# Performance work log

Hardware: AMD Instinct MI355X
Metric: run time of the kernel (lower is better)

The kernel has to match this reference:

```python
import jax, jax.numpy as jnp
import numpy as np

N_EMBD = 384
N_HEAD = 6
HEAD_SIZE = N_EMBD // N_HEAD
D_FF = 4 * N_EMBD
LN_EPS = 1e-3  # keras LayerNormalization default epsilon


def setup_inputs() -> dict:
    key = jax.random.key(0)
    ks = jax.random.split(key, 12)
    B, T = 4, 2048
    s = 1.0 / np.sqrt(N_EMBD)
    return {
        "x": jax.random.normal(ks[0], (B, T, N_EMBD), dtype=jnp.float32),
        "Wq": jax.random.normal(ks[1], (N_EMBD, N_EMBD), dtype=jnp.float32) * s,
        "Wk": jax.random.normal(ks[2], (N_EMBD, N_EMBD), dtype=jnp.float32) * s,
        "Wv": jax.random.normal(ks[3], (N_EMBD, N_EMBD), dtype=jnp.float32) * s,
        "Wo": jax.random.normal(ks[4], (N_EMBD, N_EMBD), dtype=jnp.float32) * s,
        "bo": jnp.zeros((N_EMBD,), dtype=jnp.float32),
        "W1": jax.random.normal(ks[5], (N_EMBD, D_FF), dtype=jnp.float32) * s,
        "b1": jnp.zeros((D_FF,), dtype=jnp.float32),
        "W2": jax.random.normal(ks[6], (D_FF, N_EMBD), dtype=jnp.float32) * (1.0 / np.sqrt(D_FF)),
        "b2": jnp.zeros((N_EMBD,), dtype=jnp.float32),
        "g1": jnp.ones((N_EMBD,), dtype=jnp.float32),
        "be1": jnp.zeros((N_EMBD,), dtype=jnp.float32),
        "g2": jnp.ones((N_EMBD,), dtype=jnp.float32),
        "be2": jnp.zeros((N_EMBD,), dtype=jnp.float32),
    }


def _layer_norm(x, gamma, beta):
    mu = jnp.mean(x, axis=-1, keepdims=True)
    var = jnp.mean(jnp.square(x - mu), axis=-1, keepdims=True)
    return (x - mu) * jax.lax.rsqrt(var + LN_EPS) * gamma + beta


def _block(x, Wq, Wk, Wv, Wo, bo, W1, b1, W2, b2, g1, be1, g2, be2):
    B, T, C = x.shape
    H, D = N_HEAD, HEAD_SIZE
    q = (x @ Wq).reshape(B, T, H, D).transpose(0, 2, 1, 3)  # [B,H,T,D]
    k = (x @ Wk).reshape(B, T, H, D).transpose(0, 2, 1, 3)
    v = (x @ Wv).reshape(B, T, H, D).transpose(0, 2, 1, 3)
    scores = jnp.einsum("bhqd,bhkd->bhqk", q, k) / jnp.sqrt(jnp.float32(D))
    causal = jnp.tril(jnp.ones((T, T), dtype=bool))
    scores = jnp.where(causal, scores, jnp.float32(-1e9))
    attn = jax.nn.softmax(scores, axis=-1)  # dropout is identity at inference
    out = jnp.einsum("bhqk,bhkd->bhqd", attn, v)
    out = out.transpose(0, 2, 1, 3).reshape(B, T, H * D)
    y = out @ Wo + bo
    x = _layer_norm(x + y, g1, be1)
    y = jax.nn.relu(x @ W1 + b1) @ W2 + b2
    return _layer_norm(x + y, g2, be2)


def reference(x, Wq, Wk, Wv, Wo, bo, W1, b1, W2, b2, g1, be1, g2, be2):
    return _block(x, Wq, Wk, Wv, Wo, bo, W1, b1, W2, b2, g1, be1, g2, be2)
```

## Files before the change

kernel.cpp:

```cpp
#include <hip/hip_runtime.h>

#define C_DIM  384
#define HEADS  6
#define HD     64
#define FF_DIM 1536
#define LN_EPS 1e-3f
#define TSEQ   2048
#define BATCH  4
#define LOG2E  1.4426950408889634f

typedef __attribute__((ext_vector_type(4))) float          f32x4;
typedef __attribute__((ext_vector_type(4))) float          float4_t;
typedef __attribute__((ext_vector_type(8))) short          bfrag;
typedef __attribute__((ext_vector_type(4))) unsigned short ushort4_t;
typedef __attribute__((ext_vector_type(8))) unsigned short ushort8_t;

__device__ inline unsigned short f2bf(float f) {
    unsigned int u = __builtin_bit_cast(unsigned int, f);
    u += 0x7fff + ((u >> 16) & 1);
    return (unsigned short)(u >> 16);
}

__device__ inline void gload_lds16(const void* g, void* l) {
    __builtin_amdgcn_global_load_lds(
        (const __attribute__((address_space(1))) unsigned int*)g,
        (__attribute__((address_space(3))) unsigned int*)l,
        16, 0, 0);
}

__global__ __launch_bounds__(256)
void transpose_w4(const float* __restrict__ Wq, const float* __restrict__ Wk,
                  const float* __restrict__ Wv, const float* __restrict__ Wo,
                  unsigned short* __restrict__ Dq, unsigned short* __restrict__ Dk,
                  unsigned short* __restrict__ Dv, unsigned short* __restrict__ Do_)
{
    __shared__ float tile[32][33];
    const int z = blockIdx.z;
    const float* W = z == 0 ? Wq : (z == 1 ? Wk : (z == 2 ? Wv : Wo));
    unsigned short* D = z == 0 ? Dq : (z == 1 ? Dk : (z == 2 ? Dv : Do_));
    const int tx = threadIdx.x, ty = threadIdx.y;
    const int n0 = blockIdx.x * 32, k0 = blockIdx.y * 32;
    #pragma unroll
    for (int i = 0; i < 32; i += 8)
        tile[ty + i][tx] = W[(size_t)(k0 + ty + i) * C_DIM + n0 + tx];
    __syncthreads();
    #pragma unroll
    for (int i = 0; i < 32; i += 8)
        D[(size_t)(n0 + ty + i) * C_DIM + k0 + tx] = f2bf(tile[tx][ty + i]);
}

__global__ __launch_bounds__(256)
void transpose_w(const float* __restrict__ W, unsigned short* __restrict__ Wt, int K, int N)
{
    __shared__ float tile[32][33];
    const int tx = threadIdx.x, ty = threadIdx.y;
    const int n0 = blockIdx.x * 32, k0 = blockIdx.y * 32;
    #pragma unroll
    for (int i = 0; i < 32; i += 8)
        tile[ty + i][tx] = W[(size_t)(k0 + ty + i) * N + n0 + tx];
    __syncthreads();
    #pragma unroll
    for (int i = 0; i < 32; i += 8)
        Wt[(size_t)(n0 + ty + i) * K + k0 + tx] = f2bf(tile[tx][ty + i]);
}

__global__ __launch_bounds__(256)
void cvt_f32_bf16_x4(const float* __restrict__ in, unsigned short* __restrict__ out, int n4)
{
    int i = blockIdx.x * 256 + threadIdx.x;
    if (i >= n4) return;
    float4_t v = ((const float4_t*)in)[i];
    ushort4_t o = { f2bf(v.x), f2bf(v.y), f2bf(v.z), f2bf(v.w) };
    ((ushort4_t*)out)[i] = o;
}

__global__ __launch_bounds__(256)
void vtrans_kernel(const unsigned short* __restrict__ qkv, unsigned short* __restrict__ vt)
{
    __shared__ unsigned short tile[32][34];
    const int tx = threadIdx.x, ty = threadIdx.y;
    const int bh = blockIdx.z, b = bh / HEADS, h = bh % HEADS;
    const int t0 = blockIdx.x * 32, d0 = blockIdx.y * 32;
    #pragma unroll
    for (int i = 0; i < 32; i += 8)
        tile[ty + i][tx] = qkv[(size_t)(b * TSEQ + t0 + ty + i) * 1152 + 2 * C_DIM + h * HD + d0 + tx];
    __syncthreads();
    #pragma unroll
    for (int i = 0; i < 32; i += 8)
        vt[((size_t)bh * HD + d0 + ty + i) * TSEQ + t0 + tx] = tile[tx][ty + i];
}

template<int OBF16, int BIAS, int RELU>
__global__ __launch_bounds__(256)
void gemm_lds(const unsigned short* __restrict__ A, const unsigned short* __restrict__ Bt,
              const float* __restrict__ bias, void* __restrict__ Cv,
              int M, int N, int K)
{
    __shared__ __align__(16) unsigned short As[16 * 512];
    __shared__ __align__(16) unsigned short Bs[16 * 512];

    const int t = threadIdx.x, lane = t & 63, w = t >> 6;
    const int ln16 = lane & 15, hi16 = lane >> 4;
    const int wr = w >> 1, wc = w & 1;
    const int row0 = blockIdx.y * 128, col0 = blockIdx.x * 128;

    f32x4 acc[4][4] = {};

    for (int k0 = 0; k0 < K; k0 += 64) {
        #pragma unroll
        for (int i = 0; i < 4; ++i) {
            const int f  = w * 4 + i;
            const int ks = f >> 3, rf = f & 7;
            const int row = rf * 16 + ln16;
            const int kc  = k0 + ks * 32 + hi16 * 8;
            gload_lds16(&A [(size_t)(row0 + row) * K + kc], &As[f * 512]);
            gload_lds16(&Bt[(size_t)(col0 + row) * K + kc], &Bs[f * 512]);
        }
        __syncthreads();
        #pragma unroll
        for (int ks = 0; ks < 2; ++ks) {
            bfrag a[4], b[4];
            #pragma unroll
            for (int i = 0; i < 4; ++i)
                a[i] = *(const bfrag*)&As[(ks * 8 + wr * 4 + i) * 512 + lane * 8];
            #pragma unroll
            for (int j = 0; j < 4; ++j)
                b[j] = *(const bfrag*)&Bs[(ks * 8 + wc * 4 + j) * 512 + lane * 8];
            #pragma unroll
            for (int i = 0; i < 4; ++i)
                #pragma unroll
                for (int j = 0; j < 4; ++j)
                    acc[i][j] = __builtin_amdgcn_mfma_f32_16x16x32_bf16(a[i], b[j], acc[i][j], 0, 0, 0);
        }
        __syncthreads();
    }

    #pragma unroll
    for (int j = 0; j < 4; ++j) {
        const int col = col0 + wc * 64 + j * 16 + ln16;
        const float bv = BIAS ? bias[col] : 0.0f;
        #pragma unroll
        for (int i = 0; i < 4; ++i) {
            #pragma unroll
            for (int e = 0; e < 4; ++e) {
                const int row = row0 + wr * 64 + i * 16 + hi16 * 4 + e;
                float v = acc[i][j][e] + bv;
                if (RELU) v = fmaxf(v, 0.0f);
                if (OBF16) ((unsigned short*)Cv)[(size_t)row * N + col] = f2bf(v);
                else       ((float*)Cv)[(size_t)row * N + col] = v;
            }
        }
    }
}

__global__ __launch_bounds__(64)
void attn_kernel(const unsigned short* __restrict__ qkv,
                 const unsigned short* __restrict__ vt,
                 unsigned short* __restrict__ att)
{
    __shared__ __align__(16) unsigned short Ps[32][72];
    const int lane = threadIdx.x;
    const int ln16 = lane & 15, hi16 = lane >> 4;
    const int bid = blockIdx.x;
    const int xcd = bid & 7;
    const int i2  = bid >> 3;
    const int bh  = xcd * 3 + (i2 >> 6);
    const int qw  = 63 - (i2 & 63);
    const int b   = bh / HEADS, h = bh % HEADS;
    const int tok0 = qw * 32;
    const size_t qrow0 = (size_t)b * TSEQ;

    bfrag qf[2][2];
    #pragma unroll
    for (int rf = 0; rf < 2; ++rf)
        #pragma unroll
        for (int ks = 0; ks < 2; ++ks)
            qf[rf][ks] = *(const bfrag*)&qkv[(qrow0 + tok0 + rf * 16 + ln16) * 1152 + h * HD + ks * 32 + hi16 * 8];

    f32x4 acc[2][4] = {};
    float mrow[2][4], lrow[2][4];
    #pragma unroll
    for (int rf = 0; rf < 2; ++rf)
        #pragma unroll
        for (int e = 0; e < 4; ++e) { mrow[rf][e] = -1e30f; lrow[rf][e] = 0.0f; }

    const int NT = (qw >> 1) + 1;
    const unsigned short* Kbase = qkv + qrow0 * 1152 + C_DIM + h * HD;
    const unsigned short* Vbase = vt + (size_t)bh * HD * TSEQ;

    bfrag kf[4][2];
    #pragma unroll
    for (int jt = 0; jt < 4; ++jt)
        #pragma unroll
        for (int ks = 0; ks < 2; ++ks)
            kf[jt][ks] = *(const bfrag*)&Kbase[(size_t)(jt * 16 + ln16) * 1152 + ks * 32 + hi16 * 8];

    for (int kt = 0; kt < NT; ++kt) {
        f32x4 sf[2][4] = {};
        #pragma unroll
        for (int jt = 0; jt < 4; ++jt)
            #pragma unroll
            for (int ks = 0; ks < 2; ++ks) {
                sf[0][jt] = __builtin_amdgcn_mfma_f32_16x16x32_bf16(qf[0][ks], kf[jt][ks], sf[0][jt], 0, 0, 0);
                sf[1][jt] = __builtin_amdgcn_mfma_f32_16x16x32_bf16(qf[1][ks], kf[jt][ks], sf[1][jt], 0, 0, 0);
            }

        bfrag vf[4][2];
        #pragma unroll
        for (int dt = 0; dt < 4; ++dt)
            #pragma unroll
            for (int ks = 0; ks < 2; ++ks)
                vf[dt][ks] = *(const bfrag*)&Vbase[(size_t)(dt * 16 + ln16) * TSEQ + kt * 64 + ks * 32 + hi16 * 8];

        const bool last = (kt == NT - 1);
        float p[2][4][4];
        #pragma unroll
        for (int rf = 0; rf < 2; ++rf)
            #pragma unroll
            for (int jt = 0; jt < 4; ++jt)
                #pragma unroll
                for (int e = 0; e < 4; ++e) {
                    float sv = sf[rf][jt][e] * (0.125f * LOG2E);
                    if (last) {
                        const int key = kt * 64 + jt * 16 + ln16;
                        const int row = tok0 + rf * 16 + hi16 * 4 + e;
                        if (key > row) sv = -1e30f;
                    }
                    p[rf][jt][e] = sv;
                }

        float lmax[2][4];
        bool need = false;
        #pragma unroll
        for (int rf = 0; rf < 2; ++rf)
            #pragma unroll
            for (int e = 0; e < 4; ++e) {
                float mx = fmaxf(fmaxf(p[rf][0][e], p[rf][1][e]), fmaxf(p[rf][2][e], p[rf][3][e]));
                lmax[rf][e] = mx;
                need = need || (mx > mrow[rf][e] + 8.0f);
            }
        if (__any(need)) {
            #pragma unroll
            for (int rf = 0; rf < 2; ++rf)
                #pragma unroll
                for (int e = 0; e < 4; ++e) {
                    float rm = lmax[rf][e];
                    rm = fmaxf(rm, __shfl_xor(rm, 1));
                    rm = fmaxf(rm, __shfl_xor(rm, 2));
                    rm = fmaxf(rm, __shfl_xor(rm, 4));
                    rm = fmaxf(rm, __shfl_xor(rm, 8));
                    const float mn = fmaxf(mrow[rf][e], rm);
                    const float corr = exp2f(mrow[rf][e] - mn);
                    mrow[rf][e] = mn;
                    lrow[rf][e] *= corr;
                    #pragma unroll
                    for (int dt = 0; dt < 4; ++dt) acc[rf][dt][e] *= corr;
                }
        }

        if (kt + 1 < NT) {
            const unsigned short* Kn = Kbase + (size_t)(kt + 1) * 64 * 1152;
            #pragma unroll
            for (int jt = 0; jt < 4; ++jt)
                #pragma unroll
                for (int ks = 0; ks < 2; ++ks)
                    kf[jt][ks] = *(const bfrag*)&Kn[(size_t)(jt * 16 + ln16) * 1152 + ks * 32 + hi16 * 8];
        }

        #pragma unroll
        for (int rf = 0; rf < 2; ++rf)
            #pragma unroll
            for (int jt = 0; jt < 4; ++jt)
                #pragma unroll
                for (int e = 0; e < 4; ++e) {
                    const float pe = exp2f(p[rf][jt][e] - mrow[rf][e]);
                    lrow[rf][e] += pe;
                    Ps[rf * 16 + hi16 * 4 + e][jt * 16 + ln16] = f2bf(pe);
                }

        bfrag pf[2][2];
        #pragma unroll
        for (int rf = 0; rf < 2; ++rf)
            #pragma unroll
            for (int ks = 0; ks < 2; ++ks)
                pf[rf][ks] = *(const bfrag*)&Ps[rf * 16 + ln16][ks * 32 + hi16 * 8];
        #pragma unroll
        for (int ks = 0; ks < 2; ++ks)
            #pragma unroll
            for (int rf = 0; rf < 2; ++rf)
                #pragma unroll
                for (int dt = 0; dt < 4; ++dt)
                    acc[rf][dt] = __builtin_amdgcn_mfma_f32_16x16x32_bf16(pf[rf][ks], vf[dt][ks], acc[rf][dt], 0, 0, 0);
    }

    #pragma unroll
    for (int rf = 0; rf < 2; ++rf)
        #pragma unroll
        for (int e = 0; e < 4; ++e) {
            float l = lrow[rf][e];
            l += __shfl_xor(l, 1);
            l += __shfl_xor(l, 2);
            l += __shfl_xor(l, 4);
            l += __shfl_xor(l, 8);
            const float inv = 1.0f / l;
            const size_t row = qrow0 + tok0 + rf * 16 + hi16 * 4 + e;
            #pragma unroll
            for (int dt = 0; dt < 4; ++dt)
                att[row * C_DIM + h * HD + dt * 16 + ln16] = f2bf(acc[rf][dt][e] * inv);
        }
}

template<int WB>
__global__ __launch_bounds__(256)
void ln_residual_kernel(const float* __restrict__ A, const float* __restrict__ R,
                        const float* __restrict__ gamma, const float* __restrict__ beta,
                        float* __restrict__ out, unsigned short* __restrict__ outb, int Mrows)
{
    const int lane = threadIdx.x & 63;
    const int wv   = threadIdx.x >> 6;
    const int row  = blockIdx.x * 4 + wv;
    if (row >= Mrows) return;
    const size_t off = (size_t)row * C_DIM;

    float v[6];
    float sum = 0.0f;
    #pragma unroll
    for (int j = 0; j < 6; ++j) {
        const int c = lane + 64 * j;
        v[j] = A[off + c] + R[off + c];
        sum += v[j];
    }
    #pragma unroll
    for (int o = 1; o < 64; o <<= 1) sum += __shfl_xor(sum, o);
    const float mu = sum * (1.0f / C_DIM);

    float sq = 0.0f;
    #pragma unroll
    for (int j = 0; j < 6; ++j) { const float d = v[j] - mu; sq = fmaf(d, d, sq); }
    #pragma unroll
    for (int o = 1; o < 64; o <<= 1) sq += __shfl_xor(sq, o);
    const float rstd = rsqrtf(sq * (1.0f / C_DIM) + LN_EPS);

    #pragma unroll
    for (int j = 0; j < 6; ++j) {
        const int c = lane + 64 * j;
        const float r = (v[j] - mu) * rstd * gamma[c] + beta[c];
        out[off + c] = r;
        if (WB) outb[off + c] = f2bf(r);
    }
}

extern "C" void kernel_launch(void* const* d_in, const int* in_sizes, int n_in,
                              void* d_out, int out_size, void* d_ws, size_t ws_size,
                              hipStream_t stream)
{
    const float* x   = (const float*)d_in[0];
    const float* Wq  = (const float*)d_in[1];
    const float* Wk  = (const float*)d_in[2];
    const float* Wv  = (const float*)d_in[3];
    const float* Wo  = (const float*)d_in[4];
    const float* bo  = (const float*)d_in[5];
    const float* W1  = (const float*)d_in[6];
    const float* b1  = (const float*)d_in[7];
    const float* W2  = (const float*)d_in[8];
    const float* b2  = (const float*)d_in[9];
    const float* g1  = (const float*)d_in[10];
    const float* be1 = (const float*)d_in[11];
    const float* g2  = (const float*)d_in[12];
    const float* be2 = (const float*)d_in[13];
    float* out = (float*)d_out;

    const int M = BATCH * TSEQ;
    const size_t MC = (size_t)M * C_DIM;

    char* ws = (char*)d_ws;
    unsigned short* qkv = (unsigned short*)ws;
    unsigned short* vt  = (unsigned short*)(ws + (size_t)M*1152*2);
    unsigned short* att = (unsigned short*)(ws + (size_t)M*1152*2 + (size_t)BATCH*HEADS*HD*TSEQ*2);
    unsigned short* h1  = (unsigned short*)ws;
    char* p2 = ws + (size_t)M*1152*2 + (size_t)BATCH*HEADS*HD*TSEQ*2 + MC*2;
    unsigned short* xb  = (unsigned short*)p2;
    float* y   = (float*)(p2 + MC*2);
    float* x1  = (float*)(p2 + MC*2 + MC*4);
    unsigned short* x1b = (unsigned short*)(p2 + MC*2 + 2*MC*4);
    char* p3 = p2 + MC*2 + 2*MC*4 + MC*2;
    unsigned short* Wqkv_t = (unsigned short*)p3;
    unsigned short* Wo_t   = Wqkv_t + (size_t)3*C_DIM*C_DIM;
    unsigned short* W1_t   = Wo_t   + (size_t)C_DIM*C_DIM;
    unsigned short* W2_t   = W1_t   + (size_t)FF_DIM*C_DIM;

    dim3 b256(256), b328(32, 8);

    transpose_w4<<<dim3(C_DIM/32, C_DIM/32, 4), b328, 0, stream>>>(
        Wq, Wk, Wv, Wo,
        Wqkv_t, Wqkv_t + (size_t)C_DIM*C_DIM, Wqkv_t + (size_t)2*C_DIM*C_DIM, Wo_t);
    transpose_w<<<dim3(FF_DIM/32, C_DIM/32), b328, 0, stream>>>(W1, W1_t, C_DIM, FF_DIM);
    transpose_w<<<dim3(C_DIM/32, FF_DIM/32), b328, 0, stream>>>(W2, W2_t, FF_DIM, C_DIM);

    cvt_f32_bf16_x4<<<dim3((MC/4 + 255)/256), b256, 0, stream>>>(x, xb, (int)(MC/4));

    gemm_lds<1, 0, 0><<<dim3(3*C_DIM/128, M/128), b256, 0, stream>>>(
        xb, Wqkv_t, nullptr, qkv, M, 3*C_DIM, C_DIM);

    vtrans_kernel<<<dim3(TSEQ/32, HD/32, BATCH*HEADS), b328, 0, stream>>>(qkv, vt);

    attn_kernel<<<dim3(BATCH*HEADS*64), dim3(64), 0, stream>>>(qkv, vt, att);

    gemm_lds<0, 1, 0><<<dim3(C_DIM/128, M/128), b256, 0, stream>>>(
        att, Wo_t, bo, y, M, C_DIM, C_DIM);

    ln_residual_kernel<1><<<dim3(M/4), b256, 0, stream>>>(x, y, g1, be1, x1, x1b, M);

    gemm_lds<1, 1, 1><<<dim3(FF_DIM/128, M/128), b256, 0, stream>>>(
        x1b, W1_t, b1, h1, M, FF_DIM, C_DIM);

    gemm_lds<0, 1, 0><<<dim3(C_DIM/128, M/128), b256, 0, stream>>>(
        h1, W2_t, b2, y, M, C_DIM, FF_DIM);

    ln_residual_kernel<0><<<dim3(M/4), b256, 0, stream>>>(x1, y, g2, be2, out, nullptr, M);
}
```

Measured before the change: 217.3 us.

## Split causal attention over key chunks and merge partials in a combine kernel

Attention work for each query tile is split into up to four key chunks of eight tiles each, and each chunk runs as its own workgroup. Chunks write unnormalized bf16 partial outputs plus per-row max and sum, and a new combine kernel merges them with log-sum-exp rescaling. This evens out the long causal rows and raises the number of workgroups, at the cost of an extra launch and partial-result traffic. The softmax scale (1/8·log2e) is also folded into the Q columns in the QKV GEMM epilogue, removing a multiply per score.

```diff
diff --git a/kernel.cpp b/kernel.cpp
--- a/kernel.cpp
+++ b/kernel.cpp
@@ -8,6 +8,7 @@
 #define TSEQ   2048
 #define BATCH  4
 #define LOG2E  1.4426950408889634f
+#define QK_SCALE 0.18033688011112042f
 
 typedef __attribute__((ext_vector_type(4))) float          f32x4;
 typedef __attribute__((ext_vector_type(4))) float          float4_t;
@@ -90,7 +91,7 @@
         vt[((size_t)bh * HD + d0 + ty + i) * TSEQ + t0 + tx] = tile[tx][ty + i];
 }
 
-template<int OBF16, int BIAS, int RELU>
+template<int OBF16, int BIAS, int RELU, int QSCALE>
 __global__ __launch_bounds__(256)
 void gemm_lds(const unsigned short* __restrict__ A, const unsigned short* __restrict__ Bt,
               const float* __restrict__ bias, void* __restrict__ Cv,
@@ -139,6 +140,7 @@
     for (int j = 0; j < 4; ++j) {
         const int col = col0 + wc * 64 + j * 16 + ln16;
         const float bv = BIAS ? bias[col] : 0.0f;
+        const float sc = (QSCALE && col < C_DIM) ? QK_SCALE : 1.0f;
         #pragma unroll
         for (int i = 0; i < 4; ++i) {
             #pragma unroll
@@ -146,6 +148,7 @@
                 const int row = row0 + wr * 64 + i * 16 + hi16 * 4 + e;
                 float v = acc[i][j][e] + bv;
                 if (RELU) v = fmaxf(v, 0.0f);
+                if (QSCALE) v *= sc;
                 if (OBF16) ((unsigned short*)Cv)[(size_t)row * N + col] = f2bf(v);
                 else       ((float*)Cv)[(size_t)row * N + col] = v;
             }
@@ -156,16 +159,26 @@
 __global__ __launch_bounds__(64)
 void attn_kernel(const unsigned short* __restrict__ qkv,
                  const unsigned short* __restrict__ vt,
-                 unsigned short* __restrict__ att)
+                 unsigned short* __restrict__ att,
+                 unsigned short* __restrict__ pacc,
+                 float* __restrict__ pml)
 {
     __shared__ __align__(16) unsigned short Ps[32][72];
     const int lane = threadIdx.x;
     const int ln16 = lane & 15, hi16 = lane >> 4;
     const int bid = blockIdx.x;
     const int xcd = bid & 7;
-    const int i2  = bid >> 3;
-    const int bh  = xcd * 3 + (i2 >> 6);
-    const int qw  = 63 - (i2 & 63);
+    const int r   = bid >> 3;
+    const int bh  = xcd * 3 + (r >> 8);
+    const int rr  = r & 255;
+    const int qw  = 63 - (rr >> 2);
+    const int ck  = rr & 3;
+    const int NT  = (qw >> 1) + 1;
+    const int nck = (NT + 7) >> 3;
+    if (ck >= nck) return;
+    const int kt0 = ck * 8;
+    const int kte = min(kt0 + 8, NT);
+
     const int b   = bh / HEADS, h = bh % HEADS;
     const int tok0 = qw * 32;
     const size_t qrow0 = (size_t)b * TSEQ;
@@ -184,7 +197,6 @@
         #pragma unroll
         for (int e = 0; e < 4; ++e) { mrow[rf][e] = -1e30f; lrow[rf][e] = 0.0f; }
 
-    const int NT = (qw >> 1) + 1;
     const unsigned short* Kbase = qkv + qrow0 * 1152 + C_DIM + h * HD;
     const unsigned short* Vbase = vt + (size_t)bh * HD * TSEQ;
 
@@ -193,9 +205,9 @@
     for (int jt = 0; jt < 4; ++jt)
         #pragma unroll
         for (int ks = 0; ks < 2; ++ks)
-            kf[jt][ks] = *(const bfrag*)&Kbase[(size_t)(jt * 16 + ln16) * 1152 + ks * 32 + hi16 * 8];
-
-    for (int kt = 0; kt < NT; ++kt) {
+            kf[jt][ks] = *(const bfrag*)&Kbase[(size_t)(kt0 * 64 + jt * 16 + ln16) * 1152 + ks * 32 + hi16 * 8];
+
+    for (int kt = kt0; kt < kte; ++kt) {
         f32x4 sf[2][4] = {};
         #pragma unroll
         for (int jt = 0; jt < 4; ++jt)
@@ -220,7 +232,7 @@
             for (int jt = 0; jt < 4; ++jt)
                 #pragma unroll
                 for (int e = 0; e < 4; ++e) {
-                    float sv = sf[rf][jt][e] * (0.125f * LOG2E);
+                    float sv = sf[rf][jt][e];
                     if (last) {
                         const int key = kt * 64 + jt * 16 + ln16;
                         const int row = tok0 + rf * 16 + hi16 * 4 + e;
@@ -258,7 +270,7 @@
                 }
         }
 
-        if (kt + 1 < NT) {
+        if (kt + 1 < kte) {
             const unsigned short* Kn = Kbase + (size_t)(kt + 1) * 64 * 1152;
             #pragma unroll
             for (int jt = 0; jt < 4; ++jt)
@@ -293,6 +305,7 @@
                     acc[rf][dt] = __builtin_amdgcn_mfma_f32_16x16x32_bf16(pf[rf][ks], vf[dt][ks], acc[rf][dt], 0, 0, 0);
     }
 
+    float lsum[2][4];
     #pragma unroll
     for (int rf = 0; rf < 2; ++rf)
         #pragma unroll
@@ -302,12 +315,86 @@
             l += __shfl_xor(l, 2);
             l += __shfl_xor(l, 4);
             l += __shfl_xor(l, 8);
-            const float inv = 1.0f / l;
-            const size_t row = qrow0 + tok0 + rf * 16 + hi16 * 4 + e;
+            lsum[rf][e] = l;
+        }
+
+    if (nck == 1) {
+        #pragma unroll
+        for (int rf = 0; rf < 2; ++rf)
+            #pragma unroll
+            for (int e = 0; e < 4; ++e) {
+                const float inv = 1.0f / lsum[rf][e];
+                const size_t row = qrow0 + tok0 + rf * 16 + hi16 * 4 + e;
+                #pragma unroll
+                for (int dt = 0; dt < 4; ++dt)
+                    att[row * C_DIM + h * HD + dt * 16 + ln16] = f2bf(acc[rf][dt][e] * inv);
+            }
+    } else {
+        const int sidx = bh * 48 + (qw - 16);
+        const size_t pb = (size_t)sidx * 4 + ck;
+        #pragma unroll
+        for (int rf = 0; rf < 2; ++rf)
             #pragma unroll
             for (int dt = 0; dt < 4; ++dt)
-                att[row * C_DIM + h * HD + dt * 16 + ln16] = f2bf(acc[rf][dt][e] * inv);
-        }
+                #pragma unroll
+                for (int e = 0; e < 4; ++e) {
+                    const int row = rf * 16 + hi16 * 4 + e;
+                    pacc[(pb * 32 + row) * 64 + dt * 16 + ln16] = f2bf(acc[rf][dt][e]);
+                }
+        if (ln16 == 0) {
+            #pragma unroll
+            for (int rf = 0; rf < 2; ++rf)
+                #pragma unroll
+                for (int e = 0; e < 4; ++e) {
+                    const int row = rf * 16 + hi16 * 4 + e;
+                    pml[pb * 64 + row * 2 + 0] = mrow[rf][e];
+                    pml[pb * 64 + row * 2 + 1] = lsum[rf][e];
+                }
+        }
+    }
+}
+
+__global__ __launch_bounds__(256)
+void attn_combine(const unsigned short* __restrict__ pacc,
+                  const float* __restrict__ pml,
+                  unsigned short* __restrict__ att)
+{
+    const int sidx = blockIdx.x;
+    const int bh = sidx / 48;
+    const int qw = 16 + (sidx % 48);
+    const int b = bh / HEADS, h = bh % HEADS;
+    const int NT = (qw >> 1) + 1;
+    const int nck = (NT + 7) >> 3;
+    const int tid = threadIdx.x;
+    const int row = tid >> 3;
+    const int d0  = (tid & 7) * 8;
+
+    float m[4], l[4];
+    float M = -1e30f;
+    for (int c = 0; c < nck; ++c) {
+        m[c] = pml[((size_t)sidx * 4 + c) * 64 + row * 2 + 0];
+        l[c] = pml[((size_t)sidx * 4 + c) * 64 + row * 2 + 1];
+        M = fmaxf(M, m[c]);
+    }
+    float L = 0.0f, wsc[4];
+    for (int c = 0; c < nck; ++c) { wsc[c] = exp2f(m[c] - M); L = fmaf(l[c], wsc[c], L); }
+    const float invL = 1.0f / L;
+
+    float o[8] = {};
+    for (int c = 0; c < nck; ++c) {
+        ushort8_t a = *(const ushort8_t*)&pacc[(((size_t)sidx * 4 + c) * 32 + row) * 64 + d0];
+        const float w = wsc[c];
+        #pragma unroll
+        for (int k = 0; k < 8; ++k) {
+            const float av = __builtin_bit_cast(float, (unsigned int)a[k] << 16);
+            o[k] = fmaf(av, w, o[k]);
+        }
+    }
+    ushort8_t rv;
+    #pragma unroll
+    for (int k = 0; k < 8; ++k) rv[k] = f2bf(o[k] * invL);
+    const size_t grow = (size_t)b * TSEQ + qw * 32 + row;
+    *(ushort8_t*)&att[grow * C_DIM + h * HD + d0] = rv;
 }
 
 template<int WB>
@@ -389,6 +476,9 @@
     unsigned short* W1_t   = Wo_t   + (size_t)C_DIM*C_DIM;
     unsigned short* W2_t   = W1_t   + (size_t)FF_DIM*C_DIM;
 
+    unsigned short* pacc = (unsigned short*)p2;
+    float* pml = (float*)(p2 + (size_t)4608 * 32 * 64 * 2);
+
     dim3 b256(256), b328(32, 8);
 
     transpose_w4<<<dim3(C_DIM/32, C_DIM/32, 4), b328, 0, stream>>>(
@@ -399,22 +489,23 @@
 
     cvt_f32_bf16_x4<<<dim3((MC/4 + 255)/256), b256, 0, stream>>>(x, xb, (int)(MC/4));
 
-    gemm_lds<1, 0, 0><<<dim3(3*C_DIM/128, M/128), b256, 0, stream>>>(
+    gemm_lds<1, 0, 0, 1><<<dim3(3*C_DIM/128, M/128), b256, 0, stream>>>(
         xb, Wqkv_t, nullptr, qkv, M, 3*C_DIM, C_DIM);
 
     vtrans_kernel<<<dim3(TSEQ/32, HD/32, BATCH*HEADS), b328, 0, stream>>>(qkv, vt);
 
-    attn_kernel<<<dim3(BATCH*HEADS*64), dim3(64), 0, stream>>>(qkv, vt, att);
-
-    gemm_lds<0, 1, 0><<<dim3(C_DIM/128, M/128), b256, 0, stream>>>(
+    attn_kernel<<<dim3(6144), dim3(64), 0, stream>>>(qkv, vt, att, pacc, pml);
+    attn_combine<<<dim3(1152), b256, 0, stream>>>(pacc, pml, att);
+
+    gemm_lds<0, 1, 0, 0><<<dim3(C_DIM/128, M/128), b256, 0, stream>>>(
         att, Wo_t, bo, y, M, C_DIM, C_DIM);
 
     ln_residual_kernel<1><<<dim3(M/4), b256, 0, stream>>>(x, y, g1, be1, x1, x1b, M);
 
-    gemm_lds<1, 1, 1><<<dim3(FF_DIM/128, M/128), b256, 0, stream>>>(
+    gemm_lds<1, 1, 1, 0><<<dim3(FF_DIM/128, M/128), b256, 0, stream>>>(
         x1b, W1_t, b1, h1, M, FF_DIM, C_DIM);
 
-    gemm_lds<0, 1, 0><<<dim3(C_DIM/128, M/128), b256, 0, stream>>>(
+    gemm_lds<0, 1, 0, 0><<<dim3(C_DIM/128, M/128), b256, 0, stream>>>(
         h1, W2_t, b2, y, M, C_DIM, FF_DIM);
 
     ln_residual_kernel<0><<<dim3(M/4), b256, 0, stream>>>(x1, y, g2, be2, out, nullptr, M);
```

New measurement: 253.1 us. 1.16x slower.

## Pack four attention waves per block and fold QK scale into QKV GEMM

Applied to the files above, without the earlier changes.

The attention kernel now runs four independent 64-lane waves per 256-thread block, each with its own P tile in shared memory. Blocks drop from 1536 to 384, and each block covers four consecutive query windows of one head. Separately, the softmax scale (1/8·log2e) is now applied to the Q columns in the QKV GEMM epilogue, which removes a multiply per score in the attention inner loop. The risks are that waves in one block have uneven causal lengths, so the block waits for its longest wave, and that Q is rounded to bf16 after scaling.

```diff
diff --git a/kernel.cpp b/kernel.cpp
--- a/kernel.cpp
+++ b/kernel.cpp
@@ -8,6 +8,7 @@
 #define TSEQ   2048
 #define BATCH  4
 #define LOG2E  1.4426950408889634f
+#define QK_SCALE 0.18033688011112042f
 
 typedef __attribute__((ext_vector_type(4))) float          f32x4;
 typedef __attribute__((ext_vector_type(4))) float          float4_t;
@@ -90,7 +91,7 @@
         vt[((size_t)bh * HD + d0 + ty + i) * TSEQ + t0 + tx] = tile[tx][ty + i];
 }
 
-template<int OBF16, int BIAS, int RELU>
+template<int OBF16, int BIAS, int RELU, int QSCALE>
 __global__ __launch_bounds__(256)
 void gemm_lds(const unsigned short* __restrict__ A, const unsigned short* __restrict__ Bt,
               const float* __restrict__ bias, void* __restrict__ Cv,
@@ -139,6 +140,7 @@
     for (int j = 0; j < 4; ++j) {
         const int col = col0 + wc * 64 + j * 16 + ln16;
         const float bv = BIAS ? bias[col] : 0.0f;
+        const float sc = (QSCALE && col < C_DIM) ? QK_SCALE : 1.0f;
         #pragma unroll
         for (int i = 0; i < 4; ++i) {
             #pragma unroll
@@ -146,6 +148,7 @@
                 const int row = row0 + wr * 64 + i * 16 + hi16 * 4 + e;
                 float v = acc[i][j][e] + bv;
                 if (RELU) v = fmaxf(v, 0.0f);
+                if (QSCALE) v *= sc;
                 if (OBF16) ((unsigned short*)Cv)[(size_t)row * N + col] = f2bf(v);
                 else       ((float*)Cv)[(size_t)row * N + col] = v;
             }
@@ -153,22 +156,25 @@
     }
 }
 
-__global__ __launch_bounds__(64)
+__global__ __launch_bounds__(256)
 void attn_kernel(const unsigned short* __restrict__ qkv,
                  const unsigned short* __restrict__ vt,
                  unsigned short* __restrict__ att)
 {
-    __shared__ __align__(16) unsigned short Ps[32][72];
-    const int lane = threadIdx.x;
+    __shared__ __align__(16) unsigned short Ps[4][32][72];
+    const int lane = threadIdx.x & 63;
+    const int wid  = threadIdx.x >> 6;
     const int ln16 = lane & 15, hi16 = lane >> 4;
     const int bid = blockIdx.x;
     const int xcd = bid & 7;
-    const int i2  = bid >> 3;
-    const int bh  = xcd * 3 + (i2 >> 6);
-    const int qw  = 63 - (i2 & 63);
+    const int j   = bid >> 3;
+    const int bh  = xcd * 3 + (j >> 4);
+    const int qg  = j & 15;
+    const int qw  = 63 - (qg * 4 + wid);
     const int b   = bh / HEADS, h = bh % HEADS;
     const int tok0 = qw * 32;
     const size_t qrow0 = (size_t)b * TSEQ;
+    const int NT = (qw >> 1) + 1;
 
     bfrag qf[2][2];
     #pragma unroll
@@ -184,7 +190,6 @@
         #pragma unroll
         for (int e = 0; e < 4; ++e) { mrow[rf][e] = -1e30f; lrow[rf][e] = 0.0f; }
 
-    const int NT = (qw >> 1) + 1;
     const unsigned short* Kbase = qkv + qrow0 * 1152 + C_DIM + h * HD;
     const unsigned short* Vbase = vt + (size_t)bh * HD * TSEQ;
 
@@ -220,7 +225,7 @@
             for (int jt = 0; jt < 4; ++jt)
                 #pragma unroll
                 for (int e = 0; e < 4; ++e) {
-                    float sv = sf[rf][jt][e] * (0.125f * LOG2E);
+                    float sv = sf[rf][jt][e];
                     if (last) {
                         const int key = kt * 64 + jt * 16 + ln16;
                         const int row = tok0 + rf * 16 + hi16 * 4 + e;
@@ -275,7 +280,7 @@
                 for (int e = 0; e < 4; ++e) {
                     const float pe = exp2f(p[rf][jt][e] - mrow[rf][e]);
                     lrow[rf][e] += pe;
-                    Ps[rf * 16 + hi16 * 4 + e][jt * 16 + ln16] = f2bf(pe);
+                    Ps[wid][rf * 16 + hi16 * 4 + e][jt * 16 + ln16] = f2bf(pe);
                 }
 
         bfrag pf[2][2];
@@ -283,7 +288,7 @@
         for (int rf = 0; rf < 2; ++rf)
             #pragma unroll
             for (int ks = 0; ks < 2; ++ks)
-                pf[rf][ks] = *(const bfrag*)&Ps[rf * 16 + ln16][ks * 32 + hi16 * 8];
+                pf[rf][ks] = *(const bfrag*)&Ps[wid][rf * 16 + ln16][ks * 32 + hi16 * 8];
         #pragma unroll
         for (int ks = 0; ks < 2; ++ks)
             #pragma unroll
@@ -399,22 +404,22 @@
 
     cvt_f32_bf16_x4<<<dim3((MC/4 + 255)/256), b256, 0, stream>>>(x, xb, (int)(MC/4));
 
-    gemm_lds<1, 0, 0><<<dim3(3*C_DIM/128, M/128), b256, 0, stream>>>(
+    gemm_lds<1, 0, 0, 1><<<dim3(3*C_DIM/128, M/128), b256, 0, stream>>>(
         xb, Wqkv_t, nullptr, qkv, M, 3*C_DIM, C_DIM);
 
     vtrans_kernel<<<dim3(TSEQ/32, HD/32, BATCH*HEADS), b328, 0, stream>>>(qkv, vt);
 
-    attn_kernel<<<dim3(BATCH*HEADS*64), dim3(64), 0, stream>>>(qkv, vt, att);
-
-    gemm_lds<0, 1, 0><<<dim3(C_DIM/128, M/128), b256, 0, stream>>>(
+    attn_kernel<<<dim3(384), b256, 0, stream>>>(qkv, vt, att);
+
+    gemm_lds<0, 1, 0, 0><<<dim3(C_DIM/128, M/128), b256, 0, stream>>>(
         att, Wo_t, bo, y, M, C_DIM, C_DIM);
 
     ln_residual_kernel<1><<<dim3(M/4), b256, 0, stream>>>(x, y, g1, be1, x1, x1b, M);
 
-    gemm_lds<1, 1, 1><<<dim3(FF_DIM/128, M/128), b256, 0, stream>>>(
+    gemm_lds<1, 1, 1, 0><<<dim3(FF_DIM/128, M/128), b256, 0, stream>>>(
         x1b, W1_t, b1, h1, M, FF_DIM, C_DIM);
 
-    gemm_lds<0, 1, 0><<<dim3(C_DIM/128, M/128), b256, 0, stream>>>(
+    gemm_lds<0, 1, 0, 0><<<dim3(C_DIM/128, M/128), b256, 0, stream>>>(
         h1, W2_t, b2, y, M, C_DIM, FF_DIM);
 
     ln_residual_kernel<0><<<dim3(M/4), b256, 0, stream>>>(x1, y, g2, be2, out, nullptr, M);
```

Result: slower. 227.0 us (+4.5%).
